# Performance work log

Measured on AMD Instinct MI355X. Metric: run time of the kernel, lower is better.

Reference implementation:

```python
import jax, jax.numpy as jnp
import numpy as np

SCORE_THRESHOLD = 0.05
NMS_THRESHOLD = 0.5
MAX_DETECTIONS = 300


def pairwise_iou(b):
    # b: [K, 4] as (y1, x1, y2, x2). Matches tf.image.non_max_suppression IoU.
    area = (b[:, 2] - b[:, 0]) * (b[:, 3] - b[:, 1])
    tl = jnp.maximum(b[:, None, :2], b[None, :, :2])  # [K, K, 2]
    br = jnp.minimum(b[:, None, 2:], b[None, :, 2:])
    wh = jnp.clip(br - tl, 0.0)
    inter = wh[..., 0] * wh[..., 1]
    union = area[:, None] + area[None, :] - inter
    return inter / jnp.maximum(union, 1e-8)


def nms_keep(boxes, valid):
    # Greedy NMS over boxes already sorted by descending score.
    K = boxes.shape[0]
    sup = pairwise_iou(boxes) > NMS_THRESHOLD  # [K, K]
    idxs = jnp.arange(K)

    def step(kept, i):
        suppressed = jnp.any(kept & sup[i] & (idxs < i))
        kept = kept.at[i].set(valid[i] & ~suppressed)
        return kept, None

    kept, _ = jax.lax.scan(step, jnp.zeros((K,), bool), idxs)
    return kept


def filter_one_class(boxes, scores):
    # Score threshold (tf.where(scores > thr)) -> static top-K candidate set -> NMS.
    s = jnp.where(scores > SCORE_THRESHOLD, scores, -jnp.inf)
    top_s, idx = jax.lax.top_k(s, MAX_DETECTIONS)  # sorted desc
    b = boxes[idx]  # [K, 4]
    kept = nms_keep(b, jnp.isfinite(top_s))
    return b, jnp.where(kept, top_s, -jnp.inf)


def filter_image(boxes, classification):
    # boxes: [N, 4], classification: [N, C]
    C = classification.shape[1]
    # vmap the per-class filter+NMS over the class dim (class_specific_filter=True)
    per_b, per_s = jax.vmap(filter_one_class, in_axes=(None, 0))(boxes, classification.T)
    labels = jnp.broadcast_to(jnp.arange(C, dtype=jnp.int32)[:, None], per_s.shape)
    flat_b = per_b.reshape(-1, 4)
    flat_s = per_s.reshape(-1)
    flat_l = labels.reshape(-1)
    # final top-k over all surviving (class, anchor) candidates, pad invalid with -1
    top_s, top_i = jax.lax.top_k(flat_s, MAX_DETECTIONS)
    out_b = flat_b[top_i]
    out_l = flat_l[top_i]
    valid = jnp.isfinite(top_s)
    out_boxes = jnp.where(valid[:, None], out_b, -1.0)
    out_scores = jnp.where(valid, top_s, -1.0)
    out_labels = jnp.where(valid, out_l, -1)
    return out_boxes, out_scores, out_labels


def setup_inputs() -> dict:
    key = jax.random.key(0)
    k1, k2, k3 = jax.random.split(key, 3)
    B, N, C = 2, 100000, 80
    yx = jax.random.uniform(k1, (B, N, 2), jnp.float32) * 512.0
    wh = jax.random.uniform(k2, (B, N, 2), jnp.float32) * 64.0 + 1.0
    boxes = jnp.concatenate([yx, yx + wh], axis=-1)  # valid (y1,x1,y2,x2)
    classification = jax.random.uniform(k3, (B, N, C), jnp.float32)
    return {"boxes": boxes, "classification": classification}


def reference(boxes, classification):
    # map_fn over the batch dim -> vmap
    return jax.vmap(filter_image)(boxes, classification)
```

## Files before the change

kernel.cpp:

```cpp
#include <hip/hip_runtime.h>
#include <stdint.h>

#define BATCH 2
#define NANCH 100000
#define NCLS 80
#define TOPK 300
#define NSLICE (BATCH * NCLS)
#define CAND 2048
#define FLATN (NCLS * TOPK)
#define ELEMS_PER_IMG (NANCH * NCLS)
#define F4TOTAL ((BATCH * ELEMS_PER_IMG) / 4)
#define CUT 0.992f
#define CHUNK_F4 2048
#define NBLK ((F4TOTAL + CHUNK_F4 - 1) / CHUNK_F4)
#define NBPAD 2048

__device__ __forceinline__ bool iou_gt_half(float4 a, float4 b) {
#pragma clang fp contract(off)
    float areaA = (a.z - a.x) * (a.w - a.y);
    float areaB = (b.z - b.x) * (b.w - b.y);
    float ty = fmaxf(a.x, b.x);
    float tx = fmaxf(a.y, b.y);
    float by = fminf(a.z, b.z);
    float bx = fminf(a.w, b.w);
    float hh = fmaxf(by - ty, 0.0f);
    float ww = fmaxf(bx - tx, 0.0f);
    float inter = hh * ww;
    float un = (areaA + areaB) - inter;
    float iou = inter / fmaxf(un, 1e-8f);
    return iou > 0.5f;
}

__global__ __launch_bounds__(256) void k1_count(const float* __restrict__ cls,
                                                uint32_t* __restrict__ blockcnt) {
    __shared__ uint32_t cnt[NSLICE];
    const int tid = threadIdx.x, blk = blockIdx.x;
    for (int i = tid; i < NSLICE; i += 256) cnt[i] = 0;
    __syncthreads();
    const float4* p = reinterpret_cast<const float4*>(cls);
    const int base = blk * CHUNK_F4;
#pragma unroll
    for (int j = 0; j < 8; ++j) {
        int i = base + j * 256 + tid;
        if (i < F4TOTAL) {
            float4 v = p[i];
            if (v.x >= CUT || v.y >= CUT || v.z >= CUT || v.w >= CUT) {
                uint32_t eg = (uint32_t)i * 4u;
                int b = (eg >= (uint32_t)ELEMS_PER_IMG) ? 1 : 0;
                uint32_t e = eg - (uint32_t)b * (uint32_t)ELEMS_PER_IMG;
                uint32_t c = e % NCLS;
                float arr[4] = {v.x, v.y, v.z, v.w};
#pragma unroll
                for (int q = 0; q < 4; ++q)
                    if (arr[q] >= CUT) atomicAdd(&cnt[b * NCLS + (int)c + q], 1u);
            }
        }
    }
    __syncthreads();
    for (int s = tid; s < NSLICE; s += 256) blockcnt[(size_t)s * NBPAD + blk] = cnt[s];
}

__global__ __launch_bounds__(256) void k2_scan(const uint32_t* __restrict__ blockcnt,
                                               uint32_t* __restrict__ blockbase,
                                               uint32_t* __restrict__ ccount) {
    __shared__ uint32_t A[NBPAD], B[NBPAD];
    const int s = blockIdx.x, tid = threadIdx.x;
    for (int i = tid; i < NBPAD; i += 256)
        A[i] = (i >= 1 && i <= NBLK) ? blockcnt[(size_t)s * NBPAD + i - 1] : 0u;
    __syncthreads();
    uint32_t* src = A;
    uint32_t* dst = B;
    for (int off = 1; off < NBPAD; off <<= 1) {
        for (int i = tid; i < NBPAD; i += 256)
            dst[i] = src[i] + ((i >= off) ? src[i - off] : 0u);
        __syncthreads();
        uint32_t* t = src; src = dst; dst = t;
    }
    for (int i = tid; i < NBLK; i += 256) blockbase[(size_t)s * NBPAD + i] = src[i];
    if (tid == 0) ccount[s] = src[NBLK];
}

__global__ __launch_bounds__(256) void k3_emit(const float* __restrict__ cls,
                                               const uint32_t* __restrict__ blockbase,
                                               uint64_t* __restrict__ cand) {
    __shared__ uint32_t cur[NSLICE];
    const int tid = threadIdx.x, blk = blockIdx.x;
    for (int i = tid; i < NSLICE; i += 256) cur[i] = 0;
    __syncthreads();
    const float4* p = reinterpret_cast<const float4*>(cls);
    const int base = blk * CHUNK_F4;
#pragma unroll
    for (int j = 0; j < 8; ++j) {
        int i = base + j * 256 + tid;
        if (i < F4TOTAL) {
            float4 v = p[i];
            if (v.x >= CUT || v.y >= CUT || v.z >= CUT || v.w >= CUT) {
                uint32_t eg = (uint32_t)i * 4u;
                int b = (eg >= (uint32_t)ELEMS_PER_IMG) ? 1 : 0;
                uint32_t e = eg - (uint32_t)b * (uint32_t)ELEMS_PER_IMG;
                uint32_t n = e / NCLS;
                uint32_t c = e - n * NCLS;
                float arr[4] = {v.x, v.y, v.z, v.w};
#pragma unroll
                for (int q = 0; q < 4; ++q) {
                    float s = arr[q];
                    if (s >= CUT) {
                        int slice = b * NCLS + (int)c + q;
                        uint32_t off = atomicAdd(&cur[slice], 1u);
                        uint32_t pos = blockbase[(size_t)slice * NBPAD + blk] + off;
                        if (pos < CAND)
                            cand[(size_t)slice * CAND + pos] =
                                ((uint64_t)__float_as_uint(s) << 32) | (uint64_t)(~n);
                    }
                }
            }
        }
    }
}

__global__ __launch_bounds__(256) void k4_fixup(const float* __restrict__ cls,
                                                uint32_t* __restrict__ ccount,
                                                uint64_t* __restrict__ cand) {
    const int slice = blockIdx.x;
    const uint32_t cnt0 = ccount[slice];
    if (cnt0 >= (uint32_t)TOPK && cnt0 <= (uint32_t)CAND) return;
    const int b = slice / NCLS, c = slice % NCLS;
    const float* col = cls + (size_t)b * ELEMS_PER_IMG + c;
    __shared__ uint32_t h[128];
    __shared__ uint32_t nvalid;
    __shared__ int Tb;
    const int tid = threadIdx.x;
    for (int i = tid; i < 128; i += 256) h[i] = 0;
    if (tid == 0) nvalid = 0;
    __syncthreads();
    for (int i = tid; i < NANCH; i += 256) {
        float s = col[(size_t)i * NCLS];
        if (s > 0.05f) {
            int bn = min((int)(fminf(s, 0.9999999f) * 128.0f), 127);
            atomicAdd(&h[bn], 1u);
            atomicAdd(&nvalid, 1u);
        }
    }
    __syncthreads();
    if (tid == 0) {
        uint32_t need = min((uint32_t)TOPK, nvalid);
        uint32_t cum = 0;
        int T = 0;
        if (need > 0) {
            for (int d = 127; d >= 0; --d) {
                if (cum + h[d] >= need) { T = d; break; }
                cum += h[d];
            }
        } else {
            T = 128;
        }
        Tb = T;
        ccount[slice] = 0;
    }
    __syncthreads();
    const int T = Tb;
    for (int i = tid; i < NANCH; i += 256) {
        float s = col[(size_t)i * NCLS];
        if (s > 0.05f) {
            int bn = min((int)(fminf(s, 0.9999999f) * 128.0f), 127);
            if (bn >= T) {
                uint32_t slot = atomicAdd(&ccount[slice], 1u);
                if (slot < CAND)
                    cand[(size_t)slice * CAND + slot] =
                        ((uint64_t)__float_as_uint(s) << 32) | (uint64_t)(~(uint32_t)i);
            }
        }
    }
}

__global__ __launch_bounds__(512) void k5_nms(const float* __restrict__ boxes,
                                              const uint32_t* __restrict__ ccount,
                                              const uint64_t* __restrict__ cand,
                                              uint64_t* __restrict__ staged,
                                              int* __restrict__ nsel) {
    __shared__ uint64_t keys[CAND];
    __shared__ float4 box[TOPK];
    __shared__ unsigned long long rowm[TOPK][5];
    __shared__ unsigned long long kw[5];
    const int tid = threadIdx.x;
    const int slice = blockIdx.x;
    const int b = slice / NCLS, c = slice % NCLS;
    const uint32_t cnt = min(ccount[slice], (uint32_t)CAND);
    const int SN = (cnt <= 1024u) ? 1024 : 2048;
    for (int i = tid; i < SN; i += 512)
        keys[i] = (i < (int)cnt) ? cand[(size_t)slice * CAND + i] : 0ull;

    for (int k = 2; k <= SN; k <<= 1) {
        for (int j = k >> 1; j > 0; j >>= 1) {
            __syncthreads();
            for (int i = tid; i < SN; i += 512) {
                int p = i ^ j;
                if (p > i) {
                    uint64_t a = keys[i], bb = keys[p];
                    if ((a > bb) == ((i & k) == 0)) { keys[i] = bb; keys[p] = a; }
                }
            }
        }
    }
    __syncthreads();

    for (int r = tid; r < TOPK; r += 512) {
        uint64_t sk = keys[SN - 1 - r];
        uint32_t n = sk ? ~(uint32_t)sk : 0u;
        box[r] = reinterpret_cast<const float4*>(boxes)[(size_t)b * NANCH + n];
    }
    {
        unsigned long long* f = &rowm[0][0];
        for (int i = tid; i < TOPK * 5; i += 512) f[i] = 0ull;
    }
    __syncthreads();

    for (int t = tid; t < TOPK * TOPK; t += 512) {
        int r1 = t / TOPK, r2 = t - r1 * TOPK;
        if (r2 < r1) {
            if (iou_gt_half(box[r1], box[r2]))
                atomicOr(&rowm[r1][r2 >> 6], 1ull << (r2 & 63));
        }
    }
    __syncthreads();

    if (tid < 64) {
        const int l = tid;
        unsigned long long rb[5][5];
#pragma unroll
        for (int s = 0; s < 5; ++s) {
            int r = l + 64 * s;
            bool in = r < TOPK;
#pragma unroll
            for (int w = 0; w < 5; ++w) rb[s][w] = in ? rowm[r][w] : 0ull;
        }
        unsigned long long vm[5];
#pragma unroll
        for (int s = 0; s < 5; ++s) {
            int bi = l + 64 * s;
            vm[s] = __ballot((bi < TOPK) && (keys[SN - 1 - bi] != 0ull));
        }
        uint32_t S = 0;
#pragma unroll
        for (int wi = 0; wi < 5; ++wi) {
            const int tmax = (wi == 4) ? (TOPK - 256) : 64;
            unsigned long long kwc = 0ull;
            uint32_t sbit = (S >> wi) & 1u;
            for (int t = 0; t < tmax; ++t) {
                unsigned long long bal = __ballot(sbit != 0u);
                bool sup = ((bal >> t) & 1ull) != 0ull;
                bool va = ((vm[wi] >> t) & 1ull) != 0ull;
                if (va && !sup) {
                    kwc |= (1ull << t);
#pragma unroll
                    for (int s = 0; s < 5; ++s)
                        S |= ((uint32_t)((rb[s][wi] >> t) & 1ull)) << s;
                    sbit = (S >> wi) & 1u;
                }
            }
            if (l == 0) kw[wi] = kwc;
        }
    }
    __syncthreads();

    for (int r = tid; r < TOPK; r += 512) {
        uint64_t sk = keys[SN - 1 - r];
        uint32_t flat = (uint32_t)c * TOPK + (uint32_t)r;
        uint32_t n = sk ? ~(uint32_t)sk : 0u;
        bool kept = ((kw[r >> 6] >> (r & 63)) & 1ull) != 0ull;
        nsel[(size_t)b * FLATN + flat] = (int)n;
        staged[(size_t)b * FLATN + flat] =
            (kept ? ((sk & 0xFFFFFFFF00000000ull) | (uint64_t)(~flat)) : 0ull);
    }
}

__global__ __launch_bounds__(1024) void k6_final(const float* __restrict__ boxes,
                                                 const uint64_t* __restrict__ staged,
                                                 const int* __restrict__ nsel,
                                                 float* __restrict__ out) {
    __shared__ uint32_t wsum[2][16];
    __shared__ uint64_t sel[512];
    __shared__ uint64_t rankedKey[TOPK];
    __shared__ uint32_t selCount;
    const int tid = threadIdx.x;
    const int lane = tid & 63;
    const int wid = tid >> 6;
    const int b = blockIdx.x;
    const uint64_t* keys = staged + (size_t)b * FLATN;

    uint64_t kk[24];
#pragma unroll
    for (int j = 0; j < 24; ++j) {
        int i = tid + j * 1024;
        kk[j] = (i < FLATN) ? keys[i] : 0ull;
    }
    if (tid == 0) selCount = 0;
    for (int i = tid; i < 512; i += 1024) sel[i] = 0ull;
    for (int i = tid; i < TOPK; i += 1024) rankedKey[i] = 0ull;

    {
        int c = 0;
#pragma unroll
        for (int j = 0; j < 24; ++j) c += (kk[j] != 0ull) ? 1 : 0;
#pragma unroll
        for (int off = 32; off > 0; off >>= 1) c += __shfl_down(c, off);
        if (lane == 0) wsum[0][wid] = (uint32_t)c;
    }
    __syncthreads();
    uint32_t total = 0;
#pragma unroll
    for (int w = 0; w < 16; ++w) total += wsum[0][w];
    const uint32_t need = total < (uint32_t)TOPK ? total : (uint32_t)TOPK;

    uint64_t lo = 1ull, hi = ~0ull;
    int par = 1;
    for (int it = 0; it < 64; ++it) {
        uint64_t mid = lo + ((hi - lo) >> 1);
        int c = 0;
#pragma unroll
        for (int j = 0; j < 24; ++j) c += (kk[j] >= mid) ? 1 : 0;
#pragma unroll
        for (int off = 32; off > 0; off >>= 1) c += __shfl_down(c, off);
        if (lane == 0) wsum[par][wid] = (uint32_t)c;
        __syncthreads();
        uint32_t tot = 0;
#pragma unroll
        for (int w = 0; w < 16; ++w) tot += wsum[par][w];
        if (tot >= need) lo = mid; else hi = mid;
        par ^= 1;
    }
    const uint64_t thresh = lo;

    if (need > 0) {
#pragma unroll
        for (int j = 0; j < 24; ++j) {
            uint64_t v = kk[j];
            if (v >= thresh && v != 0ull) {
                uint32_t pos = atomicAdd(&selCount, 1u);
                if (pos < 512) sel[pos] = v;
            }
        }
    }
    __syncthreads();

    for (int s = tid; s < 512; s += 1024) {
        uint64_t mine = sel[s];
        if (mine != 0ull) {
            int rank = 0;
            for (int j2 = 0; j2 < 512; ++j2) rank += (sel[j2] > mine) ? 1 : 0;
            if (rank < TOPK) rankedKey[rank] = mine;
        }
    }
    __syncthreads();

    float* outBoxes = out;
    float* outScores = out + BATCH * TOPK * 4;
    float* outLabels = out + BATCH * TOPK * 4 + BATCH * TOPK;
    for (int r0 = tid; r0 < TOPK; r0 += 1024) {
        uint64_t kkv = rankedKey[r0];
        if (kkv != 0ull) {
            uint32_t flat = ~(uint32_t)kkv;
            uint32_t c = flat / TOPK;
            uint32_t n = (uint32_t)nsel[(size_t)b * FLATN + flat];
            float4 bx = reinterpret_cast<const float4*>(boxes)[(size_t)b * NANCH + n];
            reinterpret_cast<float4*>(outBoxes)[(size_t)b * TOPK + r0] = bx;
            outScores[b * TOPK + r0] = __uint_as_float((uint32_t)(kkv >> 32));
            outLabels[b * TOPK + r0] = (float)c;
        } else {
            reinterpret_cast<float4*>(outBoxes)[(size_t)b * TOPK + r0] =
                make_float4(-1.0f, -1.0f, -1.0f, -1.0f);
            outScores[b * TOPK + r0] = -1.0f;
            outLabels[b * TOPK + r0] = -1.0f;
        }
    }
}

extern "C" void kernel_launch(void* const* d_in, const int* in_sizes, int n_in,
                              void* d_out, int out_size, void* d_ws, size_t ws_size,
                              hipStream_t stream) {
    const float* boxes = (const float*)d_in[0];
    const float* cls   = (const float*)d_in[1];
    float* out = (float*)d_out;
    char* ws = (char*)d_ws;

    size_t off = 0;
    uint32_t* blockcnt = (uint32_t*)(ws + off);
    off += (size_t)NSLICE * NBPAD * 4;
    uint32_t* blockbase = (uint32_t*)(ws + off);
    off += (size_t)NSLICE * NBPAD * 4;
    uint32_t* ccount = (uint32_t*)(ws + off); off += 4096;
    uint64_t* cand = (uint64_t*)(ws + off);
    off += (size_t)NSLICE * CAND * 8;
    uint64_t* staged = (uint64_t*)(ws + off);
    off += (size_t)BATCH * FLATN * 8;
    int* nsel = (int*)(ws + off);
    off += (size_t)BATCH * FLATN * 4;

    k1_count<<<NBLK, 256, 0, stream>>>(cls, blockcnt);
    k2_scan<<<NSLICE, 256, 0, stream>>>(blockcnt, blockbase, ccount);
    k3_emit<<<NBLK, 256, 0, stream>>>(cls, blockbase, cand);
    k4_fixup<<<NSLICE, 256, 0, stream>>>(cls, ccount, cand);
    k5_nms<<<NSLICE, 512, 0, stream>>>(boxes, ccount, cand, staged, nsel);
    k6_final<<<BATCH, 1024, 0, stream>>>(boxes, staged, nsel, out);
}
```

Before: 247.5 us.

## Stage threshold hits in k1 so emit skips rereading classification scores

The count kernel now also records each block's above-cutoff hits (key and slice) in a small per-block buffer. The emit kernel scatters from that buffer instead of rereading the whole 64MB classification tensor, and falls back to a full rescan only when a block overflows the buffer. The block-offset scan is replaced by a register plus wavefront-shuffle scan, and k5_nms gets a min-blocks launch bound of 2. The cost is extra workspace and global writes of hit lists in k1.

```diff
diff --git a/kernel.cpp b/kernel.cpp
--- a/kernel.cpp
+++ b/kernel.cpp
@@ -14,6 +14,7 @@
 #define CHUNK_F4 2048
 #define NBLK ((F4TOTAL + CHUNK_F4 - 1) / CHUNK_F4)
 #define NBPAD 2048
+#define HCAP 128
 
 __device__ __forceinline__ bool iou_gt_half(float4 a, float4 b) {
 #pragma clang fp contract(off)
@@ -32,60 +33,17 @@
 }
 
 __global__ __launch_bounds__(256) void k1_count(const float* __restrict__ cls,
-                                                uint32_t* __restrict__ blockcnt) {
+                                                uint32_t* __restrict__ blockcnt,
+                                                uint32_t* __restrict__ hitcnt,
+                                                uint64_t* __restrict__ hitKey,
+                                                uint8_t* __restrict__ hitSlice) {
     __shared__ uint32_t cnt[NSLICE];
+    __shared__ uint32_t hcnt;
+    __shared__ uint64_t hK[HCAP];
+    __shared__ uint8_t hS[HCAP];
     const int tid = threadIdx.x, blk = blockIdx.x;
     for (int i = tid; i < NSLICE; i += 256) cnt[i] = 0;
-    __syncthreads();
-    const float4* p = reinterpret_cast<const float4*>(cls);
-    const int base = blk * CHUNK_F4;
-#pragma unroll
-    for (int j = 0; j < 8; ++j) {
-        int i = base + j * 256 + tid;
-        if (i < F4TOTAL) {
-            float4 v = p[i];
-            if (v.x >= CUT || v.y >= CUT || v.z >= CUT || v.w >= CUT) {
-                uint32_t eg = (uint32_t)i * 4u;
-                int b = (eg >= (uint32_t)ELEMS_PER_IMG) ? 1 : 0;
-                uint32_t e = eg - (uint32_t)b * (uint32_t)ELEMS_PER_IMG;
-                uint32_t c = e % NCLS;
-                float arr[4] = {v.x, v.y, v.z, v.w};
-#pragma unroll
-                for (int q = 0; q < 4; ++q)
-                    if (arr[q] >= CUT) atomicAdd(&cnt[b * NCLS + (int)c + q], 1u);
-            }
-        }
-    }
-    __syncthreads();
-    for (int s = tid; s < NSLICE; s += 256) blockcnt[(size_t)s * NBPAD + blk] = cnt[s];
-}
-
-__global__ __launch_bounds__(256) void k2_scan(const uint32_t* __restrict__ blockcnt,
-                                               uint32_t* __restrict__ blockbase,
-                                               uint32_t* __restrict__ ccount) {
-    __shared__ uint32_t A[NBPAD], B[NBPAD];
-    const int s = blockIdx.x, tid = threadIdx.x;
-    for (int i = tid; i < NBPAD; i += 256)
-        A[i] = (i >= 1 && i <= NBLK) ? blockcnt[(size_t)s * NBPAD + i - 1] : 0u;
-    __syncthreads();
-    uint32_t* src = A;
-    uint32_t* dst = B;
-    for (int off = 1; off < NBPAD; off <<= 1) {
-        for (int i = tid; i < NBPAD; i += 256)
-            dst[i] = src[i] + ((i >= off) ? src[i - off] : 0u);
-        __syncthreads();
-        uint32_t* t = src; src = dst; dst = t;
-    }
-    for (int i = tid; i < NBLK; i += 256) blockbase[(size_t)s * NBPAD + i] = src[i];
-    if (tid == 0) ccount[s] = src[NBLK];
-}
-
-__global__ __launch_bounds__(256) void k3_emit(const float* __restrict__ cls,
-                                               const uint32_t* __restrict__ blockbase,
-                                               uint64_t* __restrict__ cand) {
-    __shared__ uint32_t cur[NSLICE];
-    const int tid = threadIdx.x, blk = blockIdx.x;
-    for (int i = tid; i < NSLICE; i += 256) cur[i] = 0;
+    if (tid == 0) hcnt = 0;
     __syncthreads();
     const float4* p = reinterpret_cast<const float4*>(cls);
     const int base = blk * CHUNK_F4;
@@ -105,12 +63,109 @@
                 for (int q = 0; q < 4; ++q) {
                     float s = arr[q];
                     if (s >= CUT) {
-                        int slice = b * NCLS + (int)c + q;
-                        uint32_t off = atomicAdd(&cur[slice], 1u);
-                        uint32_t pos = blockbase[(size_t)slice * NBPAD + blk] + off;
-                        if (pos < CAND)
-                            cand[(size_t)slice * CAND + pos] =
-                                ((uint64_t)__float_as_uint(s) << 32) | (uint64_t)(~n);
+                        uint32_t slice = (uint32_t)(b * NCLS) + c + (uint32_t)q;
+                        atomicAdd(&cnt[slice], 1u);
+                        uint32_t idx = atomicAdd(&hcnt, 1u);
+                        if (idx < HCAP) {
+                            hK[idx] = ((uint64_t)__float_as_uint(s) << 32) | (uint64_t)(~n);
+                            hS[idx] = (uint8_t)slice;
+                        }
+                    }
+                }
+            }
+        }
+    }
+    __syncthreads();
+    for (int s = tid; s < NSLICE; s += 256) blockcnt[(size_t)s * NBPAD + blk] = cnt[s];
+    uint32_t nh = hcnt;
+    if (tid == 0) hitcnt[blk] = nh;
+    uint32_t nw = nh < (uint32_t)HCAP ? nh : (uint32_t)HCAP;
+    for (int i = tid; i < (int)nw; i += 256) {
+        hitKey[(size_t)blk * HCAP + i] = hK[i];
+        hitSlice[(size_t)blk * HCAP + i] = hS[i];
+    }
+}
+
+__global__ __launch_bounds__(256) void k2_scan(const uint32_t* __restrict__ blockcnt,
+                                               uint32_t* __restrict__ blockbase,
+                                               uint32_t* __restrict__ ccount) {
+    __shared__ uint32_t wsum[4];
+    const int s = blockIdx.x, tid = threadIdx.x;
+    const int lane = tid & 63, wid = tid >> 6;
+    uint32_t v[8], ex[8];
+    uint32_t tot = 0;
+#pragma unroll
+    for (int q = 0; q < 8; ++q) {
+        int j = tid * 8 + q;
+        v[q] = (j < NBLK) ? blockcnt[(size_t)s * NBPAD + j] : 0u;
+        ex[q] = tot;
+        tot += v[q];
+    }
+    uint32_t x = tot;
+#pragma unroll
+    for (int d = 1; d < 64; d <<= 1) {
+        uint32_t y = __shfl_up(x, d);
+        if (lane >= d) x += y;
+    }
+    if (lane == 63) wsum[wid] = x;
+    uint32_t wexcl = x - tot;
+    __syncthreads();
+    uint32_t wbase = 0;
+#pragma unroll
+    for (int w = 0; w < 4; ++w) wbase += (w < wid) ? wsum[w] : 0u;
+    uint32_t base = wbase + wexcl;
+#pragma unroll
+    for (int q = 0; q < 8; ++q) {
+        int j = tid * 8 + q;
+        if (j < NBLK) blockbase[(size_t)s * NBPAD + j] = base + ex[q];
+    }
+    if (tid == 255) ccount[s] = base + tot;
+}
+
+__global__ __launch_bounds__(128) void k3_emit(const float* __restrict__ cls,
+                                               const uint32_t* __restrict__ blockbase,
+                                               const uint32_t* __restrict__ hitcnt,
+                                               const uint64_t* __restrict__ hitKey,
+                                               const uint8_t* __restrict__ hitSlice,
+                                               uint64_t* __restrict__ cand) {
+    __shared__ uint32_t cur[NSLICE];
+    const int tid = threadIdx.x, blk = blockIdx.x;
+    for (int i = tid; i < NSLICE; i += 128) cur[i] = 0;
+    __syncthreads();
+    const uint32_t nh = hitcnt[blk];
+    if (nh <= (uint32_t)HCAP) {
+        if (tid < (int)nh) {
+            uint32_t slice = hitSlice[(size_t)blk * HCAP + tid];
+            uint64_t key = hitKey[(size_t)blk * HCAP + tid];
+            uint32_t off = atomicAdd(&cur[slice], 1u);
+            uint32_t pos = blockbase[(size_t)slice * NBPAD + blk] + off;
+            if (pos < CAND) cand[(size_t)slice * CAND + pos] = key;
+        }
+    } else {
+        const float4* p = reinterpret_cast<const float4*>(cls);
+        const int base = blk * CHUNK_F4;
+        for (int t = tid; t < CHUNK_F4; t += 128) {
+            int i = base + t;
+            if (i < F4TOTAL) {
+                float4 v = p[i];
+                if (v.x >= CUT || v.y >= CUT || v.z >= CUT || v.w >= CUT) {
+                    uint32_t eg = (uint32_t)i * 4u;
+                    int b = (eg >= (uint32_t)ELEMS_PER_IMG) ? 1 : 0;
+                    uint32_t e = eg - (uint32_t)b * (uint32_t)ELEMS_PER_IMG;
+                    uint32_t n = e / NCLS;
+                    uint32_t c = e - n * NCLS;
+                    float arr[4] = {v.x, v.y, v.z, v.w};
+#pragma unroll
+                    for (int q = 0; q < 4; ++q) {
+                        float s = arr[q];
+                        if (s >= CUT) {
+                            int slice = b * NCLS + (int)c + q;
+                            uint32_t off = atomicAdd(&cur[slice], 1u);
+                            uint32_t pos = blockbase[(size_t)slice * NBPAD + blk] + off;
+                            if (pos < CAND)
+                                cand[(size_t)slice * CAND + pos] =
+                                    ((uint64_t)__float_as_uint(s) << 32) | (uint64_t)(~n);
+                        }
                     }
                 }
             }
@@ -173,11 +228,11 @@
     }
 }
 
-__global__ __launch_bounds__(512) void k5_nms(const float* __restrict__ boxes,
-                                              const uint32_t* __restrict__ ccount,
-                                              const uint64_t* __restrict__ cand,
-                                              uint64_t* __restrict__ staged,
-                                              int* __restrict__ nsel) {
+__global__ __launch_bounds__(512, 2) void k5_nms(const float* __restrict__ boxes,
+                                                 const uint32_t* __restrict__ ccount,
+                                                 const uint64_t* __restrict__ cand,
+                                                 uint64_t* __restrict__ staged,
+                                                 int* __restrict__ nsel) {
     __shared__ uint64_t keys[CAND];
     __shared__ float4 box[TOPK];
     __shared__ unsigned long long rowm[TOPK][5];
@@ -389,6 +444,9 @@
     uint32_t* blockbase = (uint32_t*)(ws + off);
     off += (size_t)NSLICE * NBPAD * 4;
     uint32_t* ccount = (uint32_t*)(ws + off); off += 4096;
+    uint32_t* hitcnt = (uint32_t*)(ws + off); off += NBPAD * 4;
+    uint64_t* hitKey = (uint64_t*)(ws + off); off += (size_t)NBPAD * HCAP * 8;
+    uint8_t* hitSlice = (uint8_t*)(ws + off); off += (size_t)NBPAD * HCAP;
     uint64_t* cand = (uint64_t*)(ws + off);
     off += (size_t)NSLICE * CAND * 8;
     uint64_t* staged = (uint64_t*)(ws + off);
@@ -396,9 +454,9 @@
     int* nsel = (int*)(ws + off);
     off += (size_t)BATCH * FLATN * 4;
 
-    k1_count<<<NBLK, 256, 0, stream>>>(cls, blockcnt);
+    k1_count<<<NBLK, 256, 0, stream>>>(cls, blockcnt, hitcnt, hitKey, hitSlice);
     k2_scan<<<NSLICE, 256, 0, stream>>>(blockcnt, blockbase, ccount);
-    k3_emit<<<NBLK, 256, 0, stream>>>(cls, blockbase, cand);
+    k3_emit<<<NBLK, 128, 0, stream>>>(cls, blockbase, hitcnt, hitKey, hitSlice, cand);
     k4_fixup<<<NSLICE, 256, 0, stream>>>(cls, ccount, cand);
     k5_nms<<<NSLICE, 512, 0, stream>>>(boxes, ccount, cand, staged, nsel);
     k6_final<<<BATCH, 1024, 0, stream>>>(boxes, staged, nsel, out);
```

Result: faster. 235.5 us (-4.8%).
